# Optimization experiments

Hardware: AMD Instinct MI355X
Metric: run time of the kernel (lower is better)

The kernel has to match this reference:

```python
import jax, jax.numpy as jnp
import numpy as np
from jax import lax

B, L, V, EMB = 256, 256, 14, 512
K = 16  # LSH bits (capped so 2**k fits int32)


def _conv2d(x, w, b):
    # x: [B,C,H,W], w: [O,I,3,3], padding=1 -> SAME
    y = lax.conv_general_dilated(x, w, (1, 1), ((1, 1), (1, 1)),
                                 dimension_numbers=("NCHW", "OIHW", "NCHW"))
    return y + b[None, :, None, None]


def _maxpool1d(x):  # [B,C,L] -> [B,C,L//2], kernel=stride=2
    b, c, l = x.shape
    return x.reshape(b, c, l // 2, 2).max(-1)


def _branch(tokens, emb, cw, cb, lw, lb):
    # Embedding -> pool over sequence -> Conv2d(3x3,pad1) on [C, L//2, 1] -> Linear
    e = emb[tokens]                     # [B,L,512]
    e = jnp.transpose(e, (0, 2, 1))     # [B,512,L]
    e = _maxpool1d(e)[..., None]        # [B,512,L//2,1]
    e = _conv2d(e, cw, cb)              # [B,256,L//2,1]
    return e.reshape(e.shape[0], -1) @ lw + lb


def _fog_of_war(enemy_out, rand_proj):
    # lsh_hash: random projection -> sign bits -> integer representation
    bits = (enemy_out @ rand_proj > 0).astype(jnp.int32)          # [B,K]
    pow2 = 2 ** jnp.arange(K - 1, -1, -1, dtype=jnp.int32)
    integer_repr = (bits * pow2).sum(axis=1)                      # [B] (computed as in original; loop doesn't read it)
    n = integer_repr.shape[0]
    # Greedy loop: remainder starts as arange(n); all counts are 1, so argmax
    # picks the first remaining index each iteration, which is then removed.
    def step(mask, _):
        idx = jnp.argmax(mask)  # first True = smallest remaining index
        return mask.at[idx].set(False), idx
    _, order = lax.scan(step, jnp.ones((n,), jnp.bool_), None, length=n)
    return order  # == arange(n), the original's deterministic result


def setup_inputs() -> dict:
    key = jax.random.key(0)
    ks = jax.random.split(key, 18)
    s = 0.02
    return {
        "x": jax.random.randint(ks[0], (B, L), 0, V, dtype=jnp.int32),
        "enemy_emb": jax.random.normal(ks[1], (V, EMB), jnp.float32) * s,
        "enemy_conv_w": jax.random.normal(ks[2], (256, 512, 3, 3), jnp.float32) * s,
        "enemy_conv_b": jax.random.normal(ks[3], (256,), jnp.float32) * s,
        "enemy_lin_w": jax.random.normal(ks[4], (256 * (L // 2), 128), jnp.float32) * s,
        "enemy_lin_b": jax.random.normal(ks[5], (128,), jnp.float32) * s,
        "rand_proj": jax.random.normal(ks[6], (128, K), jnp.float32),
        "manip_conv_w": jax.random.normal(ks[7], (64, 128, 3, 3), jnp.float32) * s,
        "manip_conv_b": jax.random.normal(ks[8], (64,), jnp.float32) * s,
        "manip_lin_w": jax.random.normal(ks[9], (64 * (L // 2), 256), jnp.float32) * s,
        "manip_lin_b": jax.random.normal(ks[10], (256,), jnp.float32) * s,
        "friend_emb": jax.random.normal(ks[11], (V, EMB), jnp.float32) * s,
        "friend_conv_w": jax.random.normal(ks[12], (256, 512, 3, 3), jnp.float32) * s,
        "friend_conv_b": jax.random.normal(ks[13], (256,), jnp.float32) * s,
        "friend_lin1_w": jax.random.normal(ks[14], (256 * (L // 2), 128), jnp.float32) * s,
        "friend_lin1_b": jax.random.normal(ks[15], (128,), jnp.float32) * s,
        "friend_lin2_w": jax.random.normal(ks[16], (128, V), jnp.float32) * s,
        "friend_lin2_b": jax.random.normal(ks[17], (V,), jnp.float32) * s,
    }


def reference(x, enemy_emb, enemy_conv_w, enemy_conv_b, enemy_lin_w, enemy_lin_b,
              rand_proj, manip_conv_w, manip_conv_b, manip_lin_w, manip_lin_b,
              friend_emb, friend_conv_w, friend_conv_b, friend_lin1_w, friend_lin1_b,
              friend_lin2_w, friend_lin2_b):
    # enemy branch
    enemy_out = jax.nn.softmax(
        _branch(x, enemy_emb, enemy_conv_w, enemy_conv_b, enemy_lin_w, enemy_lin_b), axis=1)  # [B,128]
    # fog_of_war: LSH hash + greedy set-cover loop -> index order
    perm = _fog_of_war(enemy_out, rand_proj)  # [B] int
    # probability manipulator: Conv2d(128,64) expects [B,128,L//2,1]
    m_in = jnp.broadcast_to(enemy_out[perm][:, :, None, None], (B, 128, L // 2, 1))
    m = jax.nn.relu(_conv2d(m_in, manip_conv_w, manip_conv_b))   # [B,64,L//2,1]
    m = m.reshape(B, -1) @ manip_lin_w + manip_lin_b             # [B,256]
    # friend branch consumes manipulator output as a token sequence (Embedding needs ints)
    tokens = (jnp.floor(jnp.abs(m) * 100.0) % V).astype(jnp.int32)  # [B,256]
    f = _branch(tokens, friend_emb, friend_conv_w, friend_conv_b, friend_lin1_w, friend_lin1_b)
    f = f @ friend_lin2_w + friend_lin2_b                        # [B,14]
    return jax.nn.softmax(f, axis=1)
```

## Files before the change

kernel.cpp:

```cpp
#include <hip/hip_runtime.h>
#include <hip/hip_bf16.h>
#include <math.h>

#define BB    256
#define LL    256
#define NV    14
#define EMBD  512
#define H2    128
#define OC    256
#define NP    196
#define JD    128
#define MO    64
#define MJ    256

#define PB_CWT    256
#define PB_MANIPW 96
#define PB_LINT   64

using s16x8 = __attribute__((ext_vector_type(8))) short;
using f32x4 = __attribute__((ext_vector_type(4))) float;

static __device__ __forceinline__ unsigned short f2bf_rne(float f) {
    unsigned int u = __float_as_uint(f);
    unsigned int r = (u + 0x7FFFu + ((u >> 16) & 1u)) >> 16;
    return (unsigned short)r;
}
static __device__ __forceinline__ float bf2f(unsigned short h) {
    return __uint_as_float(((unsigned int)h) << 16);
}

__global__ void k_prep(const float* __restrict__ cw_e, const float* __restrict__ cw_f,
                       const float* __restrict__ mcw, const float* __restrict__ mlw,
                       float* __restrict__ cwT, float* __restrict__ Wc,
                       float* __restrict__ Lint) {
    __shared__ float T[48][66];
    int bid = blockIdx.x;
    int t = threadIdx.x;
    if (bid < PB_CWT) {
        int cb = bid;
        int ic = cb & 31;
        int oc = (cb >> 5) & 3;
        int br = cb >> 7;
        int i0 = ic * 16, o0 = oc * 64;
        const float* cw = br ? cw_f : cw_e;
        int ol = t >> 2, part = t & 3;
        const float* src = cw + ((size_t)(o0 + ol) * EMBD + i0) * 9 + part * 36;
        #pragma unroll
        for (int ii = 0; ii < 4; ++ii)
            #pragma unroll
            for (int kh = 0; kh < 3; ++kh)
                T[kh * 16 + part * 4 + ii][ol] = src[ii * 9 + kh * 3 + 1];
        __syncthreads();
        int lane = t & 63, r0 = t >> 6;
        for (int rr = r0; rr < 48; rr += 4) {
            int kh = rr >> 4, il = rr & 15;
            cwT[(((size_t)(br * 3 + kh)) * EMBD + i0 + il) * OC + o0 + lane] = T[rr][lane];
        }
    } else if (bid < PB_CWT + PB_MANIPW) {
        int idx = (bid - PB_CWT) * 256 + t;
        int o = idx & 63;
        int i = (idx >> 6) & 127;
        int cls = idx >> 13;
        const float* base = mcw + ((size_t)(o * 128 + i) * 3) * 3 + 1;
        float v = 0.f;
        if (cls != 2) { v += base[3]; v += base[6]; }
        else          { v += base[0]; v += base[3]; }
        if (cls == 1)   v += base[0];
        Wc[idx] = v;
    } else {
        int o = bid - (PB_CWT + PB_MANIPW);
        float s = 0.f;
        for (int h = 1; h <= 126; h++)
            s += mlw[((size_t)(o * H2 + h)) * MJ + t];
        Lint[o * 256 + t] = s;
    }
}

__global__ __launch_bounds__(256) void k_contrib(
        const float* __restrict__ emb_e, const float* __restrict__ emb_f,
        const float* __restrict__ cwT,
        const float* __restrict__ cb_e, const float* __restrict__ cb_f,
        float* __restrict__ C) {
    int bid = blockIdx.x;
    int qg = bid % 49;
    int kh = (bid / 49) % 3;
    int br = bid / 147;
    int o = threadIdx.x;
    const float* emb = br ? emb_f : emb_e;

    __shared__ float Pl[4][512];
    for (int idx = o; idx < 4 * 512; idx += 256) {
        int row = idx >> 9, col = idx & 511;
        int q = qg * 4 + row;
        int t1 = q / NV, t2 = q % NV;
        Pl[row][col] = fmaxf(emb[t1 * EMBD + col], emb[t2 * EMBD + col]);
    }
    __syncthreads();

    const float* w = cwT + ((size_t)(br * 3 + kh) * EMBD) * OC + o;
    float acc[4] = {0.f, 0.f, 0.f, 0.f};
    #pragma unroll 8
    for (int i = 0; i < 512; i++) {
        float wv = w[(size_t)i * OC];
        #pragma unroll
        for (int qq = 0; qq < 4; qq++) acc[qq] = fmaf(wv, Pl[qq][i], acc[qq]);
    }
    float cbv = (kh == 1) ? (br ? cb_f[o] : cb_e[o]) : 0.f;
    #pragma unroll
    for (int qq = 0; qq < 4; qq++)
        C[(((size_t)br * NP + qg * 4 + qq) * 3 + kh) * OC + o] = acc[qq] + cbv;
}

template <int X3, int SK>
__global__ __launch_bounds__(512) void k_gemm(
        const int* __restrict__ tok, const float* __restrict__ C,
        const float* __restrict__ lw, float* __restrict__ partial) {
    __shared__ unsigned short Ah[2][64][SK + 4];
    __shared__ unsigned short Al[X3 ? 2 : 1][X3 ? 64 : 1][X3 ? SK + 4 : 1];
    __shared__ unsigned short Bh[2][128][SK + 4];
    __shared__ unsigned short Bl[X3 ? 2 : 1][X3 ? 128 : 1][X3 ? SK + 4 : 1];

    const int h  = blockIdx.x;
    const int B0 = blockIdx.y * 64;
    const int t  = threadIdx.x;
    constexpr int NST = 256 / SK;
    constexpr int KQ  = SK / 8;
    constexpr int JW  = SK / 4;

    const int am = t >> 3;
    const int kq = (t & 7) * KQ;
    const int* tb = tok + (size_t)(B0 + am) * LL;
    const int q1 = tb[2 * h] * NV + tb[2 * h + 1];
    const float* r1 = C + ((size_t)q1 * 3 + 1) * OC + kq;
    const float* r0 = nullptr;
    const float* r2 = nullptr;
    if (h > 0)      { int q0 = tb[2 * h - 2] * NV + tb[2 * h - 1]; r0 = C + ((size_t)q0 * 3 + 0) * OC + kq; }
    if (h < H2 - 1) { int q2 = tb[2 * h + 2] * NV + tb[2 * h + 3]; r2 = C + ((size_t)q2 * 3 + 2) * OC + kq; }

    const int ko = t & (SK - 1);
    const int j0 = (t / SK) * JW;
    const float* wsrc = lw + ((size_t)ko * H2 + h) * JD + j0;

    float4 ya[SK / 32], yb[SK / 32], yc[SK / 32], wv4[SK / 16];

    auto load = [&](int s) {
        #pragma unroll
        for (int p = 0; p < SK / 32; ++p) {
            ya[p] = *(const float4*)(r1 + s * SK + 4 * p);
            if (r0) yb[p] = *(const float4*)(r0 + s * SK + 4 * p);
            else    yb[p] = make_float4(0, 0, 0, 0);
            if (r2) yc[p] = *(const float4*)(r2 + s * SK + 4 * p);
            else    yc[p] = make_float4(0, 0, 0, 0);
        }
        const float* pw = wsrc + (size_t)s * SK * H2 * JD;
        #pragma unroll
        for (int p = 0; p < SK / 16; ++p)
            wv4[p] = *(const float4*)(pw + 4 * p);
    };

    auto store = [&](int buf) {
        #pragma unroll
        for (int p = 0; p < SK / 32; ++p) {
            float y[4];
            y[0] = ya[p].x + yb[p].x + yc[p].x; y[1] = ya[p].y + yb[p].y + yc[p].y;
            y[2] = ya[p].z + yb[p].z + yc[p].z; y[3] = ya[p].w + yb[p].w + yc[p].w;
            unsigned short hi[4];
            #pragma unroll
            for (int e = 0; e < 4; ++e) hi[e] = f2bf_rne(y[e]);
            uint2 u;
            u.x = (unsigned)hi[0] | ((unsigned)hi[1] << 16);
            u.y = (unsigned)hi[2] | ((unsigned)hi[3] << 16);
            *(uint2*)&Ah[buf][am][kq + 4 * p] = u;
            if (X3) {
                unsigned short lo[4];
                #pragma unroll
                for (int e = 0; e < 4; ++e) lo[e] = f2bf_rne(y[e] - bf2f(hi[e]));
                uint2 v;
                v.x = (unsigned)lo[0] | ((unsigned)lo[1] << 16);
                v.y = (unsigned)lo[2] | ((unsigned)lo[3] << 16);
                *(uint2*)&Al[buf][am][kq + 4 * p] = v;
            }
        }
        #pragma unroll
        for (int p = 0; p < SK / 16; ++p) {
            float wf[4] = {wv4[p].x, wv4[p].y, wv4[p].z, wv4[p].w};
            #pragma unroll
            for (int e = 0; e < 4; ++e) {
                unsigned short wh = f2bf_rne(wf[e]);
                Bh[buf][j0 + p * 4 + e][ko] = wh;
                if (X3) Bl[buf][j0 + p * 4 + e][ko] = f2bf_rne(wf[e] - bf2f(wh));
            }
        }
    };

    const int lane = t & 63, wid = t >> 6;
    const int Wm = (wid >> 2) * 32;
    const int Wn = (wid & 3) * 32;
    const int fr = lane & 15;
    const int g8 = (lane >> 4) * 8;

    f32x4 acc[2][2] = {};

    auto rd8 = [&](const unsigned short* p) -> s16x8 {
        union { s16x8 v; uint2 u[2]; } tmp;
        tmp.u[0] = *(const uint2*)(p);
        tmp.u[1] = *(const uint2*)(p + 4);
        return tmp.v;
    };

    auto compute = [&](int buf) {
        #pragma unroll
        for (int kk0 = 0; kk0 < SK; kk0 += 32) {
            s16x8 a_h[2], b_h[2];
            #pragma unroll
            for (int mf = 0; mf < 2; ++mf) a_h[mf] = rd8(&Ah[buf][Wm + mf * 16 + fr][kk0 + g8]);
            #pragma unroll
            for (int nf = 0; nf < 2; ++nf) b_h[nf] = rd8(&Bh[buf][Wn + nf * 16 + fr][kk0 + g8]);
            #pragma unroll
            for (int mf = 0; mf < 2; ++mf)
                #pragma unroll
                for (int nf = 0; nf < 2; ++nf)
                    acc[mf][nf] = __builtin_amdgcn_mfma_f32_16x16x32_bf16(a_h[mf], b_h[nf], acc[mf][nf], 0, 0, 0);
            if (X3) {
                s16x8 a_l[2], b_l[2];
                #pragma unroll
                for (int mf = 0; mf < 2; ++mf) a_l[mf] = rd8(&Al[buf][Wm + mf * 16 + fr][kk0 + g8]);
                #pragma unroll
                for (int nf = 0; nf < 2; ++nf) b_l[nf] = rd8(&Bl[buf][Wn + nf * 16 + fr][kk0 + g8]);
                #pragma unroll
                for (int mf = 0; mf < 2; ++mf)
                    #pragma unroll
                    for (int nf = 0; nf < 2; ++nf) {
                        acc[mf][nf] = __builtin_amdgcn_mfma_f32_16x16x32_bf16(a_h[mf], b_l[nf], acc[mf][nf], 0, 0, 0);
                        acc[mf][nf] = __builtin_amdgcn_mfma_f32_16x16x32_bf16(a_l[mf], b_h[nf], acc[mf][nf], 0, 0, 0);
                    }
            }
        }
    };

    load(0);
    store(0);
    __syncthreads();
    for (int s = 0; s < NST; ++s) {
        if (s < NST - 1) load(s + 1);
        compute(s & 1);
        if (s < NST - 1) store((s + 1) & 1);
        __syncthreads();
    }

    float* pb = partial + (((size_t)(B0 + Wm)) * H2 + h) * JD + Wn;
    #pragma unroll
    for (int mf = 0; mf < 2; ++mf)
        #pragma unroll
        for (int nf = 0; nf < 2; ++nf)
            #pragma unroll
            for (int r = 0; r < 4; ++r) {
                int row = mf * 16 + (lane >> 4) * 4 + r;
                int col = nf * 16 + fr;
                pb[(size_t)row * H2 * JD + col] = acc[mf][nf][r];
            }
}

__global__ __launch_bounds__(256) void k_fuseE(
        const float* __restrict__ partial, const float* __restrict__ elb,
        const float* __restrict__ Wc, const float* __restrict__ mcb,
        const float* __restrict__ mlw, const float* __restrict__ Lint,
        const float* __restrict__ mlb, int* __restrict__ tokens) {
    int b = blockIdx.x, t = threadIdx.x;
    __shared__ float S[2][128];
    __shared__ float eo[128];
    __shared__ float m3[3][64];
    __shared__ float red[128];

    int j = t & 127, hh = t >> 7;
    float s = 0.f;
    const float* pbase = partial + (size_t)b * H2 * JD + j;
    for (int h = hh * 64; h < hh * 64 + 64; ++h)
        s += pbase[(size_t)h * JD];
    S[hh][j] = s;
    __syncthreads();
    if (t < 128) {
        float v = S[0][t] + S[1][t] + elb[t];
        S[0][t] = v;
        red[t] = v;
    }
    __syncthreads();
    for (int st = 64; st > 0; st >>= 1) {
        if (t < st) red[t] = fmaxf(red[t], red[t + st]);
        __syncthreads();
    }
    float mx = red[0];
    __syncthreads();
    if (t < 128) {
        float e = expf(S[0][t] - mx);
        eo[t] = e;
        red[t] = e;
    }
    __syncthreads();
    for (int st = 64; st > 0; st >>= 1) {
        if (t < st) red[t] += red[t + st];
        __syncthreads();
    }
    float inv = 1.f / red[0];
    __syncthreads();
    if (t < 128) eo[t] *= inv;
    __syncthreads();
    if (t < 192) {
        int cls = t >> 6, o = t & 63;
        float a = mcb[o];
        const float* wp = Wc + (size_t)cls * 128 * 64 + o;
        for (int i = 0; i < 128; ++i) a = fmaf(eo[i], wp[(size_t)i * 64], a);
        m3[cls][o] = fmaxf(a, 0.f);
    }
    __syncthreads();
    float a = mlb[t];
    for (int o = 0; o < MO; ++o) {
        a = fmaf(m3[0][o], mlw[((size_t)(o * H2 + 0)) * MJ + t], a);
        a = fmaf(m3[1][o], Lint[(size_t)o * MJ + t], a);
        a = fmaf(m3[2][o], mlw[((size_t)(o * H2 + 127)) * MJ + t], a);
    }
    tokens[(size_t)b * LL + t] = ((int)floorf(fabsf(a) * 100.f)) % NV;
}

__global__ __launch_bounds__(256) void k_fuseF(
        const float* __restrict__ partial, const float* __restrict__ flb1,
        const float* __restrict__ fl2, const float* __restrict__ fb2,
        float* __restrict__ outp) {
    int b = blockIdx.x, t = threadIdx.x;
    __shared__ float S[2][128];
    __shared__ float f1[128];
    __shared__ float sl[NV];
    int j = t & 127, hh = t >> 7;
    float s = 0.f;
    const float* pbase = partial + (size_t)b * H2 * JD + j;
    for (int h = hh * 64; h < hh * 64 + 64; ++h)
        s += pbase[(size_t)h * JD];
    S[hh][j] = s;
    __syncthreads();
    if (t < 128) f1[t] = S[0][t] + S[1][t] + flb1[t];
    __syncthreads();
    if (t < NV) {
        float a = fb2[t];
        for (int jj = 0; jj < 128; ++jj) a = fmaf(f1[jj], fl2[(size_t)jj * NV + t], a);
        sl[t] = a;
    }
    __syncthreads();
    if (t < NV) {
        float mx = -1e30f;
        for (int u = 0; u < NV; ++u) mx = fmaxf(mx, sl[u]);
        float ss = 0.f;
        for (int u = 0; u < NV; ++u) ss += expf(sl[u] - mx);
        outp[(size_t)b * NV + t] = expf(sl[t] - mx) / ss;
    }
}

extern "C" void kernel_launch(void* const* d_in, const int* in_sizes, int n_in,
                              void* d_out, int out_size, void* d_ws, size_t ws_size,
                              hipStream_t stream) {
    const int*   x    = (const int*)d_in[0];
    const float* eemb = (const float*)d_in[1];
    const float* ecw  = (const float*)d_in[2];
    const float* ecb  = (const float*)d_in[3];
    const float* elw  = (const float*)d_in[4];
    const float* elb  = (const float*)d_in[5];
    const float* mcw  = (const float*)d_in[7];
    const float* mcb  = (const float*)d_in[8];
    const float* mlw  = (const float*)d_in[9];
    const float* mlb  = (const float*)d_in[10];
    const float* femb = (const float*)d_in[11];
    const float* fcw  = (const float*)d_in[12];
    const float* fcb  = (const float*)d_in[13];
    const float* flw1 = (const float*)d_in[14];
    const float* flb1 = (const float*)d_in[15];
    const float* fl2  = (const float*)d_in[16];
    const float* fb2  = (const float*)d_in[17];
    float* outp = (float*)d_out;

    char* w = (char*)d_ws;
    size_t off = 0;
    auto alloc = [&](size_t bytes) {
        void* p = w + off;
        off = (off + bytes + 255) & ~(size_t)255;
        return p;
    };
    float* cwT    = (float*)alloc(2ull * 3 * EMBD * OC * 4);
    float* C      = (float*)alloc(2ull * NP * 3 * OC * 4);
    float* Wc     = (float*)alloc(3ull * 128 * 64 * 4);
    float* Lint   = (float*)alloc(64ull * MJ * 4);
    int*   tokens = (int*)alloc((size_t)BB * LL * 4);
    float* partial= (float*)alloc((size_t)BB * H2 * JD * 4);

    const float* C_e = C;
    const float* C_f = C + (size_t)NP * 3 * OC;

    k_prep<<<PB_CWT + PB_MANIPW + PB_LINT, 256, 0, stream>>>(
        ecw, fcw, mcw, mlw, cwT, Wc, Lint);
    k_contrib<<<2 * 3 * 49, 256, 0, stream>>>(eemb, femb, cwT, ecb, fcb, C);

    k_gemm<1, 32><<<dim3(H2, 4), 512, 0, stream>>>(x, C_e, elw, partial);
    k_fuseE<<<BB, 256, 0, stream>>>(partial, elb, Wc, mcb, mlw, Lint, mlb, tokens);

    k_gemm<0, 64><<<dim3(H2, 4), 512, 0, stream>>>(tokens, C_f, flw1, partial);
    k_fuseF<<<BB, 256, 0, stream>>>(partial, flb1, fl2, fb2, outp);
}
```

Before: 92.72 us.

## Retile linear GEMM: 32-row tiles, two sequence positions per block, coalesced weight loads

Each GEMM block now covers 32 batch rows and two consecutive sequence positions, accumulating both into one partial. That halves the partial buffer and the reduction work in the fuse kernels, while the grid stays at 512 blocks. Weight loads are restructured so each thread reads consecutive output columns across k, giving coalesced global reads and vectorized LDS stores instead of scattered 2-byte transposed stores. The cost is smaller M tiles, so B-tile reuse per block drops and more weight bytes are fetched per MFMA.

```diff
diff --git a/kernel.cpp b/kernel.cpp
--- a/kernel.cpp
+++ b/kernel.cpp
@@ -12,6 +12,7 @@
 #define JD    128
 #define MO    64
 #define MJ    256
+#define GH    64
 
 #define PB_CWT    256
 #define PB_MANIPW 96
@@ -111,95 +112,104 @@
         C[(((size_t)br * NP + qg * 4 + qq) * 3 + kh) * OC + o] = acc[qq] + cbv;
 }
 
-template <int X3, int SK>
+template <int X3, int SK, int NH>
 __global__ __launch_bounds__(512) void k_gemm(
         const int* __restrict__ tok, const float* __restrict__ C,
         const float* __restrict__ lw, float* __restrict__ partial) {
-    __shared__ unsigned short Ah[2][64][SK + 4];
-    __shared__ unsigned short Al[X3 ? 2 : 1][X3 ? 64 : 1][X3 ? SK + 4 : 1];
-    __shared__ unsigned short Bh[2][128][SK + 4];
-    __shared__ unsigned short Bl[X3 ? 2 : 1][X3 ? 128 : 1][X3 ? SK + 4 : 1];
-
-    const int h  = blockIdx.x;
-    const int B0 = blockIdx.y * 64;
+    constexpr int SPH = 256 / SK;
+    constexpr int U   = NH * SPH;
+    constexpr int KA  = SK / 16;
+    constexpr int KB  = SK / 4;
+    constexpr int PD  = SK + 4;
+
+    __shared__ unsigned short Ah[2][32][PD];
+    __shared__ unsigned short Al[X3 ? 2 : 1][X3 ? 32 : 1][X3 ? PD : 1];
+    __shared__ unsigned short Bh[2][128][PD];
+    __shared__ unsigned short Bl[X3 ? 2 : 1][X3 ? 128 : 1][X3 ? PD : 1];
+
+    const int hg = blockIdx.x;
+    const int h0 = hg * NH;
+    const int B0 = blockIdx.y * 32;
     const int t  = threadIdx.x;
-    constexpr int NST = 256 / SK;
-    constexpr int KQ  = SK / 8;
-    constexpr int JW  = SK / 4;
-
-    const int am = t >> 3;
-    const int kq = (t & 7) * KQ;
+
+    const int am = t >> 4;
+    const int kq = (t & 15) * KA;
     const int* tb = tok + (size_t)(B0 + am) * LL;
-    const int q1 = tb[2 * h] * NV + tb[2 * h + 1];
-    const float* r1 = C + ((size_t)q1 * 3 + 1) * OC + kq;
-    const float* r0 = nullptr;
-    const float* r2 = nullptr;
-    if (h > 0)      { int q0 = tb[2 * h - 2] * NV + tb[2 * h - 1]; r0 = C + ((size_t)q0 * 3 + 0) * OC + kq; }
-    if (h < H2 - 1) { int q2 = tb[2 * h + 2] * NV + tb[2 * h + 3]; r2 = C + ((size_t)q2 * 3 + 2) * OC + kq; }
-
-    const int ko = t & (SK - 1);
-    const int j0 = (t / SK) * JW;
-    const float* wsrc = lw + ((size_t)ko * H2 + h) * JD + j0;
-
-    float4 ya[SK / 32], yb[SK / 32], yc[SK / 32], wv4[SK / 16];
+
+    const int jb = t & 127;
+    const int kg = (t >> 7) * KB;
+
+    const float *r1, *r0, *r2;
+    const float* wbase;
+    auto setptr = [&](int h) {
+        int q1 = tb[2 * h] * NV + tb[2 * h + 1];
+        r1 = C + ((size_t)q1 * 3 + 1) * OC + kq;
+        r0 = nullptr; r2 = nullptr;
+        if (h > 0)      { int q0 = tb[2 * h - 2] * NV + tb[2 * h - 1]; r0 = C + ((size_t)q0 * 3 + 0) * OC + kq; }
+        if (h < H2 - 1) { int q2 = tb[2 * h + 2] * NV + tb[2 * h + 3]; r2 = C + ((size_t)q2 * 3 + 2) * OC + kq; }
+        wbase = lw + (size_t)h * JD + jb;
+    };
+
+    float ya[KA], ybv[KA], ycv[KA], wv[KB];
 
     auto load = [&](int s) {
         #pragma unroll
-        for (int p = 0; p < SK / 32; ++p) {
-            ya[p] = *(const float4*)(r1 + s * SK + 4 * p);
-            if (r0) yb[p] = *(const float4*)(r0 + s * SK + 4 * p);
-            else    yb[p] = make_float4(0, 0, 0, 0);
-            if (r2) yc[p] = *(const float4*)(r2 + s * SK + 4 * p);
-            else    yc[p] = make_float4(0, 0, 0, 0);
-        }
-        const float* pw = wsrc + (size_t)s * SK * H2 * JD;
-        #pragma unroll
-        for (int p = 0; p < SK / 16; ++p)
-            wv4[p] = *(const float4*)(pw + 4 * p);
+        for (int p = 0; p < KA; ++p) {
+            ya[p]  = r1[s * SK + p];
+            ybv[p] = r0 ? r0[s * SK + p] : 0.f;
+            ycv[p] = r2 ? r2[s * SK + p] : 0.f;
+        }
+        #pragma unroll
+        for (int p = 0; p < KB; ++p)
+            wv[p] = wbase[(size_t)(s * SK + kg + p) * (H2 * JD)];
     };
 
     auto store = [&](int buf) {
-        #pragma unroll
-        for (int p = 0; p < SK / 32; ++p) {
-            float y[4];
-            y[0] = ya[p].x + yb[p].x + yc[p].x; y[1] = ya[p].y + yb[p].y + yc[p].y;
-            y[2] = ya[p].z + yb[p].z + yc[p].z; y[3] = ya[p].w + yb[p].w + yc[p].w;
-            unsigned short hi[4];
-            #pragma unroll
-            for (int e = 0; e < 4; ++e) hi[e] = f2bf_rne(y[e]);
-            uint2 u;
-            u.x = (unsigned)hi[0] | ((unsigned)hi[1] << 16);
-            u.y = (unsigned)hi[2] | ((unsigned)hi[3] << 16);
-            *(uint2*)&Ah[buf][am][kq + 4 * p] = u;
+        unsigned ap[KA / 2], alp[KA / 2];
+        #pragma unroll
+        for (int p = 0; p < KA; p += 2) {
+            float y0 = ya[p] + ybv[p] + ycv[p];
+            float y1 = ya[p + 1] + ybv[p + 1] + ycv[p + 1];
+            unsigned short h0 = f2bf_rne(y0), h1 = f2bf_rne(y1);
+            ap[p / 2] = (unsigned)h0 | ((unsigned)h1 << 16);
             if (X3) {
-                unsigned short lo[4];
-                #pragma unroll
-                for (int e = 0; e < 4; ++e) lo[e] = f2bf_rne(y[e] - bf2f(hi[e]));
-                uint2 v;
-                v.x = (unsigned)lo[0] | ((unsigned)lo[1] << 16);
-                v.y = (unsigned)lo[2] | ((unsigned)lo[3] << 16);
-                *(uint2*)&Al[buf][am][kq + 4 * p] = v;
+                unsigned short l0 = f2bf_rne(y0 - bf2f(h0));
+                unsigned short l1 = f2bf_rne(y1 - bf2f(h1));
+                alp[p / 2] = (unsigned)l0 | ((unsigned)l1 << 16);
             }
         }
-        #pragma unroll
-        for (int p = 0; p < SK / 16; ++p) {
-            float wf[4] = {wv4[p].x, wv4[p].y, wv4[p].z, wv4[p].w};
-            #pragma unroll
-            for (int e = 0; e < 4; ++e) {
-                unsigned short wh = f2bf_rne(wf[e]);
-                Bh[buf][j0 + p * 4 + e][ko] = wh;
-                if (X3) Bl[buf][j0 + p * 4 + e][ko] = f2bf_rne(wf[e] - bf2f(wh));
+        if constexpr (KA == 2) {
+            *(unsigned*)&Ah[buf][am][kq] = ap[0];
+            if (X3) *(unsigned*)&Al[buf][am][kq] = alp[0];
+        } else {
+            *(uint2*)&Ah[buf][am][kq] = make_uint2(ap[0], ap[1]);
+            if (X3) *(uint2*)&Al[buf][am][kq] = make_uint2(alp[0], alp[1]);
+        }
+        unsigned bp[KB / 2], blp[KB / 2];
+        #pragma unroll
+        for (int p = 0; p < KB; p += 2) {
+            unsigned short h0 = f2bf_rne(wv[p]), h1 = f2bf_rne(wv[p + 1]);
+            bp[p / 2] = (unsigned)h0 | ((unsigned)h1 << 16);
+            if (X3) {
+                unsigned short l0 = f2bf_rne(wv[p] - bf2f(h0));
+                unsigned short l1 = f2bf_rne(wv[p + 1] - bf2f(h1));
+                blp[p / 2] = (unsigned)l0 | ((unsigned)l1 << 16);
             }
         }
+        #pragma unroll
+        for (int g = 0; g < KB / 4; ++g) {
+            *(uint2*)&Bh[buf][jb][kg + 4 * g] = make_uint2(bp[2 * g], bp[2 * g + 1]);
+            if (X3) *(uint2*)&Bl[buf][jb][kg + 4 * g] = make_uint2(blp[2 * g], blp[2 * g + 1]);
+        }
     };
 
     const int lane = t & 63, wid = t >> 6;
-    const int Wm = (wid >> 2) * 32;
+    const int Wm = (wid >> 2) * 16;
     const int Wn = (wid & 3) * 32;
     const int fr = lane & 15;
     const int g8 = (lane >> 4) * 8;
 
-    f32x4 acc[2][2] = {};
+    f32x4 acc[2] = {};
 
     auto rd8 = [&](const unsigned short* p) -> s16x8 {
         union { s16x8 v; uint2 u[2]; } tmp;
@@ -211,54 +221,52 @@
     auto compute = [&](int buf) {
         #pragma unroll
         for (int kk0 = 0; kk0 < SK; kk0 += 32) {
-            s16x8 a_h[2], b_h[2];
-            #pragma unroll
-            for (int mf = 0; mf < 2; ++mf) a_h[mf] = rd8(&Ah[buf][Wm + mf * 16 + fr][kk0 + g8]);
+            s16x8 a_h = rd8(&Ah[buf][Wm + fr][kk0 + g8]);
+            s16x8 b_h[2];
             #pragma unroll
             for (int nf = 0; nf < 2; ++nf) b_h[nf] = rd8(&Bh[buf][Wn + nf * 16 + fr][kk0 + g8]);
             #pragma unroll
-            for (int mf = 0; mf < 2; ++mf)
-                #pragma unroll
-                for (int nf = 0; nf < 2; ++nf)
-                    acc[mf][nf] = __builtin_amdgcn_mfma_f32_16x16x32_bf16(a_h[mf], b_h[nf], acc[mf][nf], 0, 0, 0);
+            for (int nf = 0; nf < 2; ++nf)
+                acc[nf] = __builtin_amdgcn_mfma_f32_16x16x32_bf16(a_h, b_h[nf], acc[nf], 0, 0, 0);
             if (X3) {
-                s16x8 a_l[2], b_l[2];
-                #pragma unroll
-                for (int mf = 0; mf < 2; ++mf) a_l[mf] = rd8(&Al[buf][Wm + mf * 16 + fr][kk0 + g8]);
+                s16x8 a_l = rd8(&Al[buf][Wm + fr][kk0 + g8]);
+                s16x8 b_l[2];
                 #pragma unroll
                 for (int nf = 0; nf < 2; ++nf) b_l[nf] = rd8(&Bl[buf][Wn + nf * 16 + fr][kk0 + g8]);
                 #pragma unroll
-                for (int mf = 0; mf < 2; ++mf)
-                    #pragma unroll
-                    for (int nf = 0; nf < 2; ++nf) {
-                        acc[mf][nf] = __builtin_amdgcn_mfma_f32_16x16x32_bf16(a_h[mf], b_l[nf], acc[mf][nf], 0, 0, 0);
-                        acc[mf][nf] = __builtin_amdgcn_mfma_f32_16x16x32_bf16(a_l[mf], b_h[nf], acc[mf][nf], 0, 0, 0);
-                    }
+                for (int nf = 0; nf < 2; ++nf) {
+                    acc[nf] = __builtin_amdgcn_mfma_f32_16x16x32_bf16(a_h, b_l[nf], acc[nf], 0, 0, 0);
+                    acc[nf] = __builtin_amdgcn_mfma_f32_16x16x32_bf16(a_l, b_h[nf], acc[nf], 0, 0, 0);
+                }
             }
         }
     };
 
+    setptr(h0);
     load(0);
     store(0);
     __syncthreads();
-    for (int s = 0; s < NST; ++s) {
-        if (s < NST - 1) load(s + 1);
-        compute(s & 1);
-        if (s < NST - 1) store((s + 1) & 1);
+    int cur = 0;
+    for (int u = 0; u < U; ++u) {
+        int un = u + 1;
+        if (un < U) {
+            if ((un % SPH) == 0) setptr(h0 + un / SPH);
+            load(un % SPH);
+        }
+        compute(cur);
+        if (un < U) store(cur ^ 1);
         __syncthreads();
-    }
-
-    float* pb = partial + (((size_t)(B0 + Wm)) * H2 + h) * JD + Wn;
+        cur ^= 1;
+    }
+
+    float* pb = partial + (((size_t)(B0 + Wm)) * GH + hg) * JD + Wn;
     #pragma unroll
-    for (int mf = 0; mf < 2; ++mf)
-        #pragma unroll
-        for (int nf = 0; nf < 2; ++nf)
-            #pragma unroll
-            for (int r = 0; r < 4; ++r) {
-                int row = mf * 16 + (lane >> 4) * 4 + r;
-                int col = nf * 16 + fr;
-                pb[(size_t)row * H2 * JD + col] = acc[mf][nf][r];
-            }
+    for (int nf = 0; nf < 2; ++nf)
+        #pragma unroll
+        for (int r = 0; r < 4; ++r) {
+            int row = (lane >> 4) * 4 + r;
+            pb[(size_t)row * GH * JD + nf * 16 + fr] = acc[nf][r];
+        }
 }
 
 __global__ __launch_bounds__(256) void k_fuseE(
@@ -274,8 +282,8 @@
 
     int j = t & 127, hh = t >> 7;
     float s = 0.f;
-    const float* pbase = partial + (size_t)b * H2 * JD + j;
-    for (int h = hh * 64; h < hh * 64 + 64; ++h)
+    const float* pbase = partial + (size_t)b * GH * JD + j;
+    for (int h = hh * 32; h < hh * 32 + 32; ++h)
         s += pbase[(size_t)h * JD];
     S[hh][j] = s;
     __syncthreads();
@@ -332,8 +340,8 @@
     __shared__ float sl[NV];
     int j = t & 127, hh = t >> 7;
     float s = 0.f;
-    const float* pbase = partial + (size_t)b * H2 * JD + j;
-    for (int h = hh * 64; h < hh * 64 + 64; ++h)
+    const float* pbase = partial + (size_t)b * GH * JD + j;
+    for (int h = hh * 32; h < hh * 32 + 32; ++h)
         s += pbase[(size_t)h * JD];
     S[hh][j] = s;
     __syncthreads();
@@ -388,7 +396,7 @@
     float* Wc     = (float*)alloc(3ull * 128 * 64 * 4);
     float* Lint   = (float*)alloc(64ull * MJ * 4);
     int*   tokens = (int*)alloc((size_t)BB * LL * 4);
-    float* partial= (float*)alloc((size_t)BB * H2 * JD * 4);
+    float* partial= (float*)alloc((size_t)BB * GH * JD * 4);
 
     const float* C_e = C;
     const float* C_f = C + (size_t)NP * 3 * OC;
@@ -397,9 +405,9 @@
         ecw, fcw, mcw, mlw, cwT, Wc, Lint);
     k_contrib<<<2 * 3 * 49, 256, 0, stream>>>(eemb, femb, cwT, ecb, fcb, C);
 
-    k_gemm<1, 32><<<dim3(H2, 4), 512, 0, stream>>>(x, C_e, elw, partial);
+    k_gemm<1, 32, 2><<<dim3(GH, 8), 512, 0, stream>>>(x, C_e, elw, partial);
     k_fuseE<<<BB, 256, 0, stream>>>(partial, elb, Wc, mcb, mlw, Lint, mlb, tokens);
 
-    k_gemm<0, 64><<<dim3(H2, 4), 512, 0, stream>>>(tokens, C_f, flw1, partial);
+    k_gemm<0, 64, 2><<<dim3(GH, 8), 512, 0, stream>>>(tokens, C_f, flw1, partial);
     k_fuseF<<<BB, 256, 0, stream>>>(partial, flb1, fl2, fb2, outp);
 }
```

Result: slower. 111.7 us (+20.5%).
